# Kernel optimization log

Measured on AMD Instinct MI355X. Metric: run time of the kernel, lower is better.

Reference implementation:

```python
import jax, jax.numpy as jnp
import numpy as np

FEA, DK, H = 512, 64, 8
B, L = 4, 2048
EPS = 1e-5


def _layernorm(x, g, b):
    mu = jnp.mean(x, axis=-1, keepdims=True)
    var = jnp.mean(jnp.square(x - mu), axis=-1, keepdims=True)
    return (x - mu) * jax.lax.rsqrt(var + EPS) * g + b


def setup_inputs() -> dict:
    key = jax.random.key(0)
    ks = jax.random.split(key, 12)
    d = {
        'qx': jax.random.normal(ks[0], (B, L, FEA), jnp.float32),
        'kx': jax.random.normal(ks[1], (B, L, FEA), jnp.float32),
        'vx': jax.random.normal(ks[2], (B, L, FEA), jnp.float32),
        'maskPAD': jax.random.randint(ks[3], (B, L, L), 0, 2, jnp.int32),
        # attention projections (stored as [in, out]); biases zero-init as in module
        'wq': jax.random.normal(ks[4], (FEA, DK * H), jnp.float32) * 0.02,
        'bq': jnp.zeros((DK * H,), jnp.float32),
        'wk': jax.random.normal(ks[5], (FEA, DK * H), jnp.float32) * 0.02,
        'bk': jnp.zeros((DK * H,), jnp.float32),
        'wv': jax.random.normal(ks[6], (FEA, DK * H), jnp.float32) * 0.02,
        'bv': jnp.zeros((DK * H,), jnp.float32),
        'wo': jax.random.normal(ks[7], (DK * H, FEA), jnp.float32) * 0.02,
        'bo': jnp.zeros((FEA,), jnp.float32),
        # FFN
        'w1': jax.random.normal(ks[8], (FEA, 4 * FEA), jnp.float32) * 0.02,
        'b1': jnp.zeros((4 * FEA,), jnp.float32),
        'w2': jax.random.normal(ks[9], (4 * FEA, FEA), jnp.float32) * 0.02,
        'b2': jnp.zeros((FEA,), jnp.float32),
        # layer norms
        'ln1_g': jnp.ones((FEA,), jnp.float32),
        'ln1_b': jnp.zeros((FEA,), jnp.float32),
        'ln2_g': jnp.ones((FEA,), jnp.float32),
        'ln2_b': jnp.zeros((FEA,), jnp.float32),
    }
    return d


def reference(qx, kx, vx, maskPAD, wq, bq, wk, bk, wv, bv, wo, bo,
              w1, b1, w2, b2, ln1_g, ln1_b, ln2_g, ln2_b):
    b, l, _ = qx.shape
    # project and split heads: [B, H, L, DK]
    q = (qx @ wq + bq).reshape(b, l, H, DK).transpose(0, 2, 1, 3)
    k = (kx @ wk + bk).reshape(b, l, H, DK).transpose(0, 2, 1, 3)
    v = (vx @ wv + bv).reshape(b, l, H, DK).transpose(0, 2, 1, 3)
    scores = jnp.einsum('bhqd,bhkd->bhqk', q, k) / np.sqrt(DK)  # [B,H,L,L]
    mask = (maskPAD == 0)[:, None, :, :]
    scores = jnp.where(mask, jnp.float32(-2 ** 15 + 1), scores)
    alpha = jax.nn.softmax(scores, axis=-1)
    z = jnp.einsum('bhqk,bhkd->bhqd', alpha, v)  # [B,H,L,DK]
    z = z.transpose(0, 2, 1, 3).reshape(b, l, H * DK)
    z = z @ wo + bo
    # post-LN FFN block (dropout = identity at inference)
    zn = _layernorm(vx + z, ln1_g, ln1_b)
    ffn = jax.nn.gelu(zn @ w1 + b1, approximate=False) @ w2 + b2
    return _layernorm(zn + ffn, ln2_g, ln2_b)
```

## Files before the change

kernel.cpp:

```cpp
#include <hip/hip_runtime.h>
#include <cstdint>


typedef __bf16 bf16;
typedef __bf16 bf16x8 __attribute__((ext_vector_type(8)));
typedef float floatx4 __attribute__((ext_vector_type(4)));

__device__ __forceinline__ floatx4 mfma_bf16(bf16x8 a, bf16x8 b, floatx4 c) {
  return __builtin_amdgcn_mfma_f32_16x16x32_bf16(a, b, c, 0, 0, 0);
}

__device__ __forceinline__ void load_lds_16(const void* g, void* l) {
  auto gp = reinterpret_cast<const void __attribute__((address_space(1)))*>(
      reinterpret_cast<uintptr_t>(g));
  auto lp = reinterpret_cast<void __attribute__((address_space(3)))*>(
      (unsigned int)reinterpret_cast<uintptr_t>(l));
  __builtin_amdgcn_global_load_lds(gp, lp, 16, 0, 0);
}

__device__ __forceinline__ float gelu_f(float x) {
  float t = 0.7978845608f * (x + 0.044715f * x * x * x);
  float e = __builtin_amdgcn_exp2f(t * 2.885390082f);
  float th = 1.0f - 2.0f * __builtin_amdgcn_rcpf(e + 1.0f);
  return 0.5f * x * (1.0f + th);
}

#define PLANE128 2064
#define PLANE64 1040
#define PSTR 72

__global__ void __launch_bounds__(256) transpose4_k(const float* __restrict__ w0,
                                                    const float* __restrict__ w1,
                                                    const float* __restrict__ w2,
                                                    const float* __restrict__ w3,
                                                    bf16* __restrict__ o0,
                                                    bf16* __restrict__ o1,
                                                    bf16* __restrict__ o2,
                                                    bf16* __restrict__ o3) {
  const float* in = (blockIdx.z == 0) ? w0 : (blockIdx.z == 1) ? w1
                    : (blockIdx.z == 2) ? w2 : w3;
  bf16* out = (blockIdx.z == 0) ? o0 : (blockIdx.z == 1) ? o1
              : (blockIdx.z == 2) ? o2 : o3;
  __shared__ float tile[32][33];
  int m0 = blockIdx.x * 32, k0 = blockIdx.y * 32;
  int tx = threadIdx.x, ty = threadIdx.y;
  for (int i = ty; i < 32; i += 8)
    tile[i][tx] = in[(size_t)(k0 + i) * 512 + m0 + tx];
  __syncthreads();
  for (int i = ty; i < 32; i += 8)
    out[(size_t)(m0 + i) * 512 + k0 + tx] = (bf16)tile[tx][i];
}

__global__ void __launch_bounds__(256) transpose_k(const float* __restrict__ in,
                                                   bf16* __restrict__ out,
                                                   int K, int M) {
  __shared__ float tile[32][33];
  int m0 = blockIdx.x * 32, k0 = blockIdx.y * 32;
  int tx = threadIdx.x, ty = threadIdx.y;
  for (int i = ty; i < 32; i += 8)
    tile[i][tx] = in[(size_t)(k0 + i) * M + m0 + tx];
  __syncthreads();
  for (int i = ty; i < 32; i += 8)
    out[(size_t)(m0 + i) * K + k0 + tx] = (bf16)tile[tx][i];
}

__global__ void __launch_bounds__(256) maskbits_k(const int* __restrict__ m,
                                                  unsigned long long* __restrict__ out) {
  int w = blockIdx.x * 4 + (threadIdx.x >> 6);
  int lane = threadIdx.x & 63;
  int v = m[(size_t)w * 64 + lane];
  unsigned long long b = __ballot(v != 0);
  if (lane == 0) out[w] = b;
}

template <int EPI>
__device__ __forceinline__ void epi_store(void* Cout, int n, int m, int M,
                                          float val) {
  if constexpr (EPI == 1) {
    int bb = n >> 11, l = n & 2047, hh = m >> 6, d = m & 63;
    ((bf16*)Cout)[((size_t)((bb * 8 + hh) * 2048 + l)) * 64 + d] = (bf16)val;
  } else if constexpr (EPI == 2) {
    int bb = n >> 11, l = n & 2047, hh = m >> 6, d = m & 63;
    ((bf16*)Cout)[((size_t)((bb * 8 + hh) * 64 + d)) * 2048 + l] = (bf16)val;
  } else if constexpr (EPI == 3) {
    ((bf16*)Cout)[(size_t)n * M + m] = (bf16)gelu_f(val);
  } else if constexpr (EPI == 4) {
    ((float*)Cout)[(size_t)n * M + m] = val;
  } else {
    ((float*)Cout)[(size_t)n * M + m] += val;
  }
}

template <int EPI, bool TALL>
__global__ void __launch_bounds__(256) gemm_bt(const bf16* __restrict__ A,
                                               const bf16* __restrict__ Bt,
                                               const float* __restrict__ bias,
                                               void* __restrict__ Cout,
                                               int M, int K, int lda, int ldb) {
  __shared__ __attribute__((aligned(16))) char As[8 * PLANE128];
  __shared__ __attribute__((aligned(16))) char Bs[TALL ? 8 * PLANE64 : 8 * PLANE128];
  int tid = threadIdx.x, wave = tid >> 6, lane = tid & 63;
  int lrow = lane & 15, quad = lane >> 4;
  int n0 = blockIdx.y * 128;
  int m0 = blockIdx.x * (TALL ? 64 : 128);
  int wr = wave >> 1, wc = wave & 1;
  floatx4 zero4 = {0.f, 0.f, 0.f, 0.f};
  constexpr int NI = TALL ? 2 : 4;
  floatx4 acc[NI][4];
#pragma unroll
  for (int i = 0; i < NI; ++i)
#pragma unroll
    for (int j = 0; j < 4; ++j) acc[i][j] = zero4;
  for (int k0 = 0; k0 < K; k0 += 64) {
    __syncthreads();
#pragma unroll
    for (int h = 0; h < 2; ++h) {
      int p = wave + 4 * h;
#pragma unroll
      for (int j = 0; j < 2; ++j) {
        int row = j * 64 + lane;
        load_lds_16(A + (size_t)(n0 + row) * lda + k0 + p * 8,
                    As + p * PLANE128 + j * 1024 + lane * 16);
      }
      if constexpr (TALL) {
        load_lds_16(Bt + (size_t)(m0 + lane) * ldb + k0 + p * 8,
                    Bs + p * PLANE64 + lane * 16);
      } else {
#pragma unroll
        for (int j = 0; j < 2; ++j) {
          int row = j * 64 + lane;
          load_lds_16(Bt + (size_t)(m0 + row) * ldb + k0 + p * 8,
                      Bs + p * PLANE128 + j * 1024 + lane * 16);
        }
      }
    }
    __syncthreads();
#pragma unroll
    for (int h = 0; h < 2; ++h) {
      int pb = h * 4 + quad;
      bf16x8 af[NI], bfr[4];
#pragma unroll
      for (int i = 0; i < NI; ++i) {
        int row = (TALL ? wave * 32 : wr * 64) + i * 16 + lrow;
        af[i] = *(const bf16x8*)(As + pb * PLANE128 + row * 16);
      }
#pragma unroll
      for (int j = 0; j < 4; ++j) {
        if constexpr (TALL)
          bfr[j] = *(const bf16x8*)(Bs + pb * PLANE64 + (j * 16 + lrow) * 16);
        else
          bfr[j] = *(const bf16x8*)(Bs + pb * PLANE128 +
                                    (wc * 64 + j * 16 + lrow) * 16);
      }
#pragma unroll
      for (int i = 0; i < NI; ++i)
#pragma unroll
        for (int j = 0; j < 4; ++j)
          acc[i][j] = mfma_bf16(af[i], bfr[j], acc[i][j]);
    }
  }
  float bv[4];
#pragma unroll
  for (int j = 0; j < 4; ++j) {
    int m = m0 + (TALL ? 0 : wc * 64) + j * 16 + lrow;
    bv[j] = (EPI == 5) ? 0.f : bias[m];
  }
#pragma unroll
  for (int i = 0; i < NI; ++i)
#pragma unroll
    for (int j = 0; j < 4; ++j)
#pragma unroll
      for (int r = 0; r < 4; ++r) {
        int n = n0 + (TALL ? wave * 32 : wr * 64) + i * 16 + quad * 4 + r;
        int m = m0 + (TALL ? 0 : wc * 64) + j * 16 + lrow;
        epi_store<EPI>(Cout, n, m, M, acc[i][j][r] + bv[j]);
      }
}

__global__ void __launch_bounds__(256) qkv_k(const float* __restrict__ qx,
                                             const float* __restrict__ kx,
                                             const float* __restrict__ vx,
                                             const bf16* __restrict__ wqT,
                                             const bf16* __restrict__ wkT,
                                             const bf16* __restrict__ wvT,
                                             const float* __restrict__ bq,
                                             const float* __restrict__ bk,
                                             const float* __restrict__ bv_,
                                             bf16* __restrict__ qh,
                                             bf16* __restrict__ kh,
                                             bf16* __restrict__ vt) {
  __shared__ __attribute__((aligned(16))) char As[8 * PLANE128];
  __shared__ __attribute__((aligned(16))) char Bs[8 * PLANE128];
  int tid = threadIdx.x, wave = tid >> 6, lane = tid & 63;
  int lrow = lane & 15, quad = lane >> 4;
  int seg = blockIdx.y >> 6;
  int n0 = (blockIdx.y & 63) * 128, m0 = blockIdx.x * 128;
  const float* Af = (seg == 0) ? qx : (seg == 1) ? kx : vx;
  const bf16* Bt = (seg == 0) ? wqT : (seg == 1) ? wkT : wvT;
  const float* bias = (seg == 0) ? bq : (seg == 1) ? bk : bv_;
  bf16* out = (seg == 0) ? qh : (seg == 1) ? kh : vt;
  int wr = wave >> 1, wc = wave & 1;
  floatx4 zero4 = {0.f, 0.f, 0.f, 0.f};
  floatx4 acc[4][4];
#pragma unroll
  for (int i = 0; i < 4; ++i)
#pragma unroll
    for (int j = 0; j < 4; ++j) acc[i][j] = zero4;
  int arow = tid >> 2, ap = tid & 3;
  for (int k0 = 0; k0 < 512; k0 += 64) {
    bf16x8 a[4];
#pragma unroll
    for (int u = 0; u < 4; ++u) {
      int row = arow + (u & 1) * 64, p = ap + (u >> 1) * 4;
      const float* src = Af + (size_t)(n0 + row) * 512 + k0 + p * 8;
      float4 x0 = *(const float4*)src;
      float4 x1 = *(const float4*)(src + 4);
      a[u][0] = (bf16)x0.x; a[u][1] = (bf16)x0.y; a[u][2] = (bf16)x0.z;
      a[u][3] = (bf16)x0.w; a[u][4] = (bf16)x1.x; a[u][5] = (bf16)x1.y;
      a[u][6] = (bf16)x1.z; a[u][7] = (bf16)x1.w;
    }
    __syncthreads();
#pragma unroll
    for (int u = 0; u < 4; ++u) {
      int row = arow + (u & 1) * 64, p = ap + (u >> 1) * 4;
      *(bf16x8*)(As + p * PLANE128 + row * 16) = a[u];
    }
#pragma unroll
    for (int h = 0; h < 2; ++h) {
      int p = wave + 4 * h;
#pragma unroll
      for (int j = 0; j < 2; ++j) {
        int row = j * 64 + lane;
        load_lds_16(Bt + (size_t)(m0 + row) * 512 + k0 + p * 8,
                    Bs + p * PLANE128 + j * 1024 + lane * 16);
      }
    }
    __syncthreads();
#pragma unroll
    for (int h = 0; h < 2; ++h) {
      int pb = h * 4 + quad;
      bf16x8 af[4], bfr[4];
#pragma unroll
      for (int t = 0; t < 4; ++t) {
        af[t] = *(const bf16x8*)(As + pb * PLANE128 + (wr * 64 + t * 16 + lrow) * 16);
        bfr[t] = *(const bf16x8*)(Bs + pb * PLANE128 + (wc * 64 + t * 16 + lrow) * 16);
      }
#pragma unroll
      for (int i = 0; i < 4; ++i)
#pragma unroll
        for (int j = 0; j < 4; ++j) acc[i][j] = mfma_bf16(af[i], bfr[j], acc[i][j]);
    }
  }
  float bvv[4];
#pragma unroll
  for (int j = 0; j < 4; ++j) bvv[j] = bias[m0 + wc * 64 + j * 16 + lrow];
#pragma unroll
  for (int i = 0; i < 4; ++i)
#pragma unroll
    for (int j = 0; j < 4; ++j)
#pragma unroll
      for (int r = 0; r < 4; ++r) {
        int n = n0 + wr * 64 + i * 16 + quad * 4 + r;
        int m = m0 + wc * 64 + j * 16 + lrow;
        float val = acc[i][j][r] + bvv[j];
        int bb = n >> 11, l = n & 2047, hh = m >> 6, d = m & 63;
        if (seg == 2)
          out[((size_t)((bb * 8 + hh) * 64 + d)) * 2048 + l] = (bf16)val;
        else
          out[((size_t)((bb * 8 + hh) * 2048 + l)) * 64 + d] = (bf16)val;
      }
}

__global__ void __launch_bounds__(256) attn_k(const bf16* __restrict__ Qh,
                                              const bf16* __restrict__ Kh,
                                              const bf16* __restrict__ Vt,
                                              const unsigned long long* __restrict__ MB,
                                              bf16* __restrict__ Z) {
  __shared__ __attribute__((aligned(16))) char Ks[8 * PLANE64];
  __shared__ __attribute__((aligned(16))) char Vs[8 * PLANE64];
  __shared__ __attribute__((aligned(16))) bf16 Ps[4][16 * PSTR];
  int qt = blockIdx.x, h = blockIdx.y, b = blockIdx.z;
  int tid = threadIdx.x, wave = tid >> 6, lane = tid & 63;
  int lrow = lane & 15, quad = lane >> 4;
  int q0 = qt * 64;
  size_t headbase = (size_t)(b * 8 + h) * 2048 * 64;

  const bf16* Qp = Qh + headbase + (size_t)(q0 + wave * 16 + lrow) * 64 + quad * 8;
  bf16x8 qf0 = *(const bf16x8*)Qp;
  bf16x8 qf1 = *(const bf16x8*)(Qp + 32);

  floatx4 zero4 = {0.f, 0.f, 0.f, 0.f};
  floatx4 o_acc[4], acc_l = zero4;
#pragma unroll
  for (int dt = 0; dt < 4; ++dt) o_acc[dt] = zero4;
  bf16x8 ones;
#pragma unroll
  for (int j = 0; j < 8; ++j) ones[j] = (bf16)1.0f;

  const bf16* Vg = Vt + headbase;
  const uint2* MBb = (const uint2*)(MB + ((size_t)b * 2048 + q0 + wave * 16) * 32);
  bf16* Pw = Ps[wave];
  const float C = 0.1803368801f;

  for (int kt = 0; kt < 32; ++kt) {
    int kk0 = kt * 64;
    const bf16* Kg = Kh + headbase + (size_t)kk0 * 64;
    __syncthreads();
#pragma unroll
    for (int j = 0; j < 2; ++j) {
      int p = wave * 2 + j;
      load_lds_16(Kg + (size_t)lane * 64 + p * 8, Ks + p * PLANE64 + lane * 16);
      load_lds_16(Vg + (size_t)lane * 2048 + kk0 + p * 8,
                  Vs + p * PLANE64 + lane * 16);
    }
    unsigned sx[4], sy[4];
#pragma unroll
    for (int r = 0; r < 4; ++r) {
      uint2 mw = MBb[(quad * 4 + r) * 32 + kt];
      sx[r] = mw.x >> lrow;
      sy[r] = mw.y >> lrow;
    }
    __syncthreads();

#pragma unroll
    for (int nt = 0; nt < 4; ++nt) {
      int R = nt * 16 + lrow;
      bf16x8 k0f = *(const bf16x8*)(Ks + quad * PLANE64 + R * 16);
      bf16x8 k1f = *(const bf16x8*)(Ks + (quad + 4) * PLANE64 + R * 16);
      floatx4 aa = zero4;
      aa = mfma_bf16(qf0, k0f, aa);
      aa = mfma_bf16(qf1, k1f, aa);
#pragma unroll
      for (int r = 0; r < 4; ++r) {
        float e = __builtin_amdgcn_exp2f(aa[r] * C);
        unsigned bit = ((nt < 2 ? sx[r] : sy[r]) >> ((nt & 1) * 16)) & 1u;
        Pw[(quad * 4 + r) * PSTR + nt * 16 + lrow] = (bf16)(bit ? e : 0.f);
      }
    }
    bf16x8 pf0 = *(const bf16x8*)(Pw + lrow * PSTR + quad * 8);
    bf16x8 pf1 = *(const bf16x8*)(Pw + lrow * PSTR + 32 + quad * 8);
    acc_l = mfma_bf16(pf0, ones, acc_l);
    acc_l = mfma_bf16(pf1, ones, acc_l);
#pragma unroll
    for (int dt = 0; dt < 4; ++dt) {
      int R = dt * 16 + lrow;
      bf16x8 v0 = *(const bf16x8*)(Vs + quad * PLANE64 + R * 16);
      bf16x8 v1 = *(const bf16x8*)(Vs + (quad + 4) * PLANE64 + R * 16);
      o_acc[dt] = mfma_bf16(pf0, v0, o_acc[dt]);
      o_acc[dt] = mfma_bf16(pf1, v1, o_acc[dt]);
    }
  }
  float lr[4];
#pragma unroll
  for (int r = 0; r < 4; ++r) lr[r] = 1.0f / acc_l[r];
#pragma unroll
  for (int dt = 0; dt < 4; ++dt)
#pragma unroll
    for (int r = 0; r < 4; ++r) {
      int qrow = q0 + wave * 16 + quad * 4 + r;
      int d = dt * 16 + lrow;
      Z[((size_t)(b * 2048 + qrow)) * 512 + h * 64 + d] = (bf16)(o_acc[dt][r] * lr[r]);
    }
}

template <bool A_BF16, bool OUT_BF16>
__global__ void __launch_bounds__(256) ln_k(const void* __restrict__ a_,
                                            const float* __restrict__ s,
                                            const float* __restrict__ g,
                                            const float* __restrict__ bta,
                                            void* __restrict__ out_) {
  int row = blockIdx.x * 4 + (threadIdx.x >> 6);
  int lane = threadIdx.x & 63;
  size_t base = (size_t)row * 512 + lane * 8;
  float x[8];
  float4 sa = *(const float4*)(s + base);
  float4 sb = *(const float4*)(s + base + 4);
  if constexpr (A_BF16) {
    bf16x8 av = *(const bf16x8*)((const bf16*)a_ + base);
    x[0] = (float)av[0] + sa.x; x[1] = (float)av[1] + sa.y;
    x[2] = (float)av[2] + sa.z; x[3] = (float)av[3] + sa.w;
    x[4] = (float)av[4] + sb.x; x[5] = (float)av[5] + sb.y;
    x[6] = (float)av[6] + sb.z; x[7] = (float)av[7] + sb.w;
  } else {
    float4 a0 = *(const float4*)((const float*)a_ + base);
    float4 a1 = *(const float4*)((const float*)a_ + base + 4);
    x[0] = a0.x + sa.x; x[1] = a0.y + sa.y; x[2] = a0.z + sa.z; x[3] = a0.w + sa.w;
    x[4] = a1.x + sb.x; x[5] = a1.y + sb.y; x[6] = a1.z + sb.z; x[7] = a1.w + sb.w;
  }
  float sum = 0.f;
#pragma unroll
  for (int i = 0; i < 8; ++i) sum += x[i];
#pragma unroll
  for (int off = 1; off < 64; off <<= 1) sum += __shfl_xor(sum, off, 64);
  float mu = sum * (1.0f / 512.0f);
  float vs = 0.f;
#pragma unroll
  for (int i = 0; i < 8; ++i) { float d = x[i] - mu; vs += d * d; }
#pragma unroll
  for (int off = 1; off < 64; off <<= 1) vs += __shfl_xor(vs, off, 64);
  float rstd = rsqrtf(vs * (1.0f / 512.0f) + 1e-5f);
  float4 g0 = *(const float4*)(g + lane * 8);
  float4 g1 = *(const float4*)(g + lane * 8 + 4);
  float4 b0 = *(const float4*)(bta + lane * 8);
  float4 b1 = *(const float4*)(bta + lane * 8 + 4);
  float gg[8] = {g0.x, g0.y, g0.z, g0.w, g1.x, g1.y, g1.z, g1.w};
  float bb[8] = {b0.x, b0.y, b0.z, b0.w, b1.x, b1.y, b1.z, b1.w};
  if constexpr (OUT_BF16) {
    bf16x8 o;
#pragma unroll
    for (int i = 0; i < 8; ++i)
      o[i] = (bf16)((x[i] - mu) * rstd * gg[i] + bb[i]);
    *(bf16x8*)((bf16*)out_ + base) = o;
  } else {
    float4 o0, o1;
    o0.x = (x[0] - mu) * rstd * gg[0] + bb[0];
    o0.y = (x[1] - mu) * rstd * gg[1] + bb[1];
    o0.z = (x[2] - mu) * rstd * gg[2] + bb[2];
    o0.w = (x[3] - mu) * rstd * gg[3] + bb[3];
    o1.x = (x[4] - mu) * rstd * gg[4] + bb[4];
    o1.y = (x[5] - mu) * rstd * gg[5] + bb[5];
    o1.z = (x[6] - mu) * rstd * gg[6] + bb[6];
    o1.w = (x[7] - mu) * rstd * gg[7] + bb[7];
    *(float4*)((float*)out_ + base) = o0;
    *(float4*)((float*)out_ + base + 4) = o1;
  }
}

extern "C" void kernel_launch(void* const* d_in, const int* in_sizes, int n_in,
                              void* d_out, int out_size, void* d_ws, size_t ws_size,
                              hipStream_t stream) {
  const float* qx = (const float*)d_in[0];
  const float* kx = (const float*)d_in[1];
  const float* vx = (const float*)d_in[2];
  const int* maskPAD = (const int*)d_in[3];
  const float* wq = (const float*)d_in[4];
  const float* bq = (const float*)d_in[5];
  const float* wk = (const float*)d_in[6];
  const float* bk = (const float*)d_in[7];
  const float* wv = (const float*)d_in[8];
  const float* bv = (const float*)d_in[9];
  const float* wo = (const float*)d_in[10];
  const float* bo = (const float*)d_in[11];
  const float* w1 = (const float*)d_in[12];
  const float* b1 = (const float*)d_in[13];
  const float* w2 = (const float*)d_in[14];
  const float* b2 = (const float*)d_in[15];
  const float* g1 = (const float*)d_in[16];
  const float* be1 = (const float*)d_in[17];
  const float* g2 = (const float*)d_in[18];
  const float* be2 = (const float*)d_in[19];

  char* w = (char*)d_ws;
  size_t off = 0;
  auto alloc = [&](size_t bytes) {
    void* p = w + off;
    off += (bytes + 255) & ~(size_t)255;
    return p;
  };
  bf16* wqT = (bf16*)alloc(512 * 512 * 2);
  bf16* wkT = (bf16*)alloc(512 * 512 * 2);
  bf16* wvT = (bf16*)alloc(512 * 512 * 2);
  bf16* woT = (bf16*)alloc(512 * 512 * 2);
  bf16* w1T = (bf16*)alloc(2048 * 512 * 2);
  bf16* w2T = (bf16*)alloc(512 * 2048 * 2);
  unsigned long long* mbits = (unsigned long long*)alloc((size_t)4 * 2048 * 32 * 8);
  bf16* qh = (bf16*)alloc((size_t)8192 * 512 * 2);
  bf16* kh = (bf16*)alloc((size_t)8192 * 512 * 2);
  bf16* vt = (bf16*)alloc((size_t)8192 * 512 * 2);
  bf16* z = (bf16*)alloc((size_t)8192 * 512 * 2);
  float* s12 = (float*)qh;
  bf16* zn = vt;
  size_t h1_bytes = (size_t)8192 * 2048 * 2;
  bool big = (off + h1_bytes) <= ws_size;
  bf16* h1 = big ? (bf16*)alloc(h1_bytes) : z;

  dim3 tb(32, 8);
  transpose4_k<<<dim3(16, 16, 4), tb, 0, stream>>>(wq, wk, wv, wo, wqT, wkT, wvT, woT);
  transpose_k<<<dim3(64, 16), tb, 0, stream>>>(w1, w1T, 512, 2048);
  transpose_k<<<dim3(16, 64), tb, 0, stream>>>(w2, w2T, 2048, 512);
  maskbits_k<<<65536, 256, 0, stream>>>(maskPAD, mbits);
  qkv_k<<<dim3(4, 192), 256, 0, stream>>>(qx, kx, vx, wqT, wkT, wvT, bq, bk, bv,
                                          qh, kh, vt);
  attn_k<<<dim3(32, 8, 4), 256, 0, stream>>>(qh, kh, vt, mbits, z);
  gemm_bt<4, true><<<dim3(8, 64), 256, 0, stream>>>(z, woT, bo, s12, 512, 512,
                                                    512, 512);
  ln_k<false, true><<<2048, 256, 0, stream>>>(vx, s12, g1, be1, zn);
  if (big) {
    gemm_bt<3, false><<<dim3(16, 64), 256, 0, stream>>>(zn, w1T, b1, h1, 2048,
                                                        512, 512, 512);
    gemm_bt<4, true><<<dim3(8, 64), 256, 0, stream>>>(h1, w2T, b2, s12, 512,
                                                      2048, 2048, 2048);
  } else {
    for (int p = 0; p < 4; ++p) {
      gemm_bt<3, true><<<dim3(8, 64), 256, 0, stream>>>(
          zn, w1T + (size_t)p * 512 * 512, b1 + p * 512, h1, 512, 512, 512, 512);
      if (p == 0)
        gemm_bt<4, true><<<dim3(8, 64), 256, 0, stream>>>(
            h1, w2T + p * 512, b2, s12, 512, 512, 512, 2048);
      else
        gemm_bt<5, true><<<dim3(8, 64), 256, 0, stream>>>(
            h1, w2T + p * 512, nullptr, s12, 512, 512, 512, 2048);
    }
  }
  ln_k<true, false><<<2048, 256, 0, stream>>>(zn, s12, g2, be2, (float*)d_out);
}
```

Before: 455.0 us.

## Pre-convert QKV inputs to bf16 and transpose attention MFMA operand order

Adds a kernel that converts qx/kx/vx to bf16 once, so a new QKV GEMM can stream the A operand into LDS with direct global-to-LDS loads instead of converting fp32 on the fly. In attention, the MFMA operands are swapped so each lane holds a row of scores, which allows one 64-bit mask word load per lane, packed bf16x4 writes of P, and vectorized Z stores. This costs an extra conversion pass and a larger workspace, and the conversion path is used only when the workspace is big enough.

Result: slower. 469.1 us (+3.1%).

```diff
diff --git a/kernel.cpp b/kernel.cpp
--- a/kernel.cpp
+++ b/kernel.cpp
@@ -3,6 +3,7 @@
 
 
 typedef __bf16 bf16;
+typedef __bf16 bf16x4 __attribute__((ext_vector_type(4)));
 typedef __bf16 bf16x8 __attribute__((ext_vector_type(8)));
 typedef float floatx4 __attribute__((ext_vector_type(4)));
 
@@ -64,6 +65,19 @@
     out[(size_t)(m0 + i) * K + k0 + tx] = (bf16)tile[tx][i];
 }
 
+__global__ void __launch_bounds__(256) cvt3_k(const float* __restrict__ a,
+                                              const float* __restrict__ b,
+                                              const float* __restrict__ c,
+                                              bf16* __restrict__ out) {
+  int seg = blockIdx.x >> 12;
+  const float* in = (seg == 0) ? a : (seg == 1) ? b : c;
+  int i = ((blockIdx.x & 4095) * 256 + threadIdx.x) * 4;
+  float4 v = *(const float4*)(in + i);
+  bf16x4 o;
+  o[0] = (bf16)v.x; o[1] = (bf16)v.y; o[2] = (bf16)v.z; o[3] = (bf16)v.w;
+  *(bf16x4*)(out + (size_t)seg * 4194304 + i) = o;
+}
+
 __global__ void __launch_bounds__(256) maskbits_k(const int* __restrict__ m,
                                                   unsigned long long* __restrict__ out) {
   int w = blockIdx.x * 4 + (threadIdx.x >> 6);
@@ -174,6 +188,83 @@
         int n = n0 + (TALL ? wave * 32 : wr * 64) + i * 16 + quad * 4 + r;
         int m = m0 + (TALL ? 0 : wc * 64) + j * 16 + lrow;
         epi_store<EPI>(Cout, n, m, M, acc[i][j][r] + bv[j]);
+      }
+}
+
+__global__ void __launch_bounds__(256) qkv2_k(const bf16* __restrict__ xall,
+                                              const bf16* __restrict__ wqT,
+                                              const bf16* __restrict__ wkT,
+                                              const bf16* __restrict__ wvT,
+                                              const float* __restrict__ bq,
+                                              const float* __restrict__ bk,
+                                              const float* __restrict__ bv_,
+                                              bf16* __restrict__ qh,
+                                              bf16* __restrict__ kh,
+                                              bf16* __restrict__ vt) {
+  __shared__ __attribute__((aligned(16))) char As[8 * PLANE128];
+  __shared__ __attribute__((aligned(16))) char Bs[8 * PLANE128];
+  int tid = threadIdx.x, wave = tid >> 6, lane = tid & 63;
+  int lrow = lane & 15, quad = lane >> 4;
+  int seg = blockIdx.y >> 6;
+  int n0 = (blockIdx.y & 63) * 128, m0 = blockIdx.x * 128;
+  const bf16* A = xall + (size_t)seg * 4194304;
+  const bf16* Bt = (seg == 0) ? wqT : (seg == 1) ? wkT : wvT;
+  const float* bias = (seg == 0) ? bq : (seg == 1) ? bk : bv_;
+  bf16* out = (seg == 0) ? qh : (seg == 1) ? kh : vt;
+  int wr = wave >> 1, wc = wave & 1;
+  floatx4 zero4 = {0.f, 0.f, 0.f, 0.f};
+  floatx4 acc[4][4];
+#pragma unroll
+  for (int i = 0; i < 4; ++i)
+#pragma unroll
+    for (int j = 0; j < 4; ++j) acc[i][j] = zero4;
+  for (int k0 = 0; k0 < 512; k0 += 64) {
+    __syncthreads();
+#pragma unroll
+    for (int h = 0; h < 2; ++h) {
+      int p = wave + 4 * h;
+#pragma unroll
+      for (int j = 0; j < 2; ++j) {
+        int row = j * 64 + lane;
+        load_lds_16(A + (size_t)(n0 + row) * 512 + k0 + p * 8,
+                    As + p * PLANE128 + j * 1024 + lane * 16);
+        load_lds_16(Bt + (size_t)(m0 + row) * 512 + k0 + p * 8,
+                    Bs + p * PLANE128 + j * 1024 + lane * 16);
+      }
+    }
+    __syncthreads();
+#pragma unroll
+    for (int h = 0; h < 2; ++h) {
+      int pb = h * 4 + quad;
+      bf16x8 af[4], bfr[4];
+#pragma unroll
+      for (int t = 0; t < 4; ++t) {
+        af[t] = *(const bf16x8*)(As + pb * PLANE128 + (wr * 64 + t * 16 + lrow) * 16);
+        bfr[t] = *(const bf16x8*)(Bs + pb * PLANE128 + (wc * 64 + t * 16 + lrow) * 16);
+      }
+#pragma unroll
+      for (int i = 0; i < 4; ++i)
+#pragma unroll
+        for (int j = 0; j < 4; ++j) acc[i][j] = mfma_bf16(af[i], bfr[j], acc[i][j]);
+    }
+  }
+  float bvv[4];
+#pragma unroll
+  for (int j = 0; j < 4; ++j) bvv[j] = bias[m0 + wc * 64 + j * 16 + lrow];
+#pragma unroll
+  for (int i = 0; i < 4; ++i)
+#pragma unroll
+    for (int j = 0; j < 4; ++j)
+#pragma unroll
+      for (int r = 0; r < 4; ++r) {
+        int n = n0 + wr * 64 + i * 16 + quad * 4 + r;
+        int m = m0 + wc * 64 + j * 16 + lrow;
+        float val = acc[i][j][r] + bvv[j];
+        int bb = n >> 11, l = n & 2047, hh = m >> 6, d = m & 63;
+        if (seg == 2)
+          out[((size_t)((bb * 8 + hh) * 64 + d)) * 2048 + l] = (bf16)val;
+        else
+          out[((size_t)((bb * 8 + hh) * 2048 + l)) * 64 + d] = (bf16)val;
       }
 }
 
@@ -278,7 +369,7 @@
                                               bf16* __restrict__ Z) {
   __shared__ __attribute__((aligned(16))) char Ks[8 * PLANE64];
   __shared__ __attribute__((aligned(16))) char Vs[8 * PLANE64];
-  __shared__ __attribute__((aligned(16))) bf16 Ps[4][16 * PSTR];
+  __shared__ __attribute__((aligned(16))) bf16 Pt[4][16 * PSTR];
   int qt = blockIdx.x, h = blockIdx.y, b = blockIdx.z;
   int tid = threadIdx.x, wave = tid >> 6, lane = tid & 63;
   int lrow = lane & 15, quad = lane >> 4;
@@ -298,8 +389,9 @@
   for (int j = 0; j < 8; ++j) ones[j] = (bf16)1.0f;
 
   const bf16* Vg = Vt + headbase;
-  const uint2* MBb = (const uint2*)(MB + ((size_t)b * 2048 + q0 + wave * 16) * 32);
-  bf16* Pw = Ps[wave];
+  const unsigned long long* MBrow =
+      MB + ((size_t)b * 2048 + q0 + wave * 16 + lrow) * 32;
+  bf16* Pw = Pt[wave];
   const float C = 0.1803368801f;
 
   for (int kt = 0; kt < 32; ++kt) {
@@ -313,13 +405,9 @@
       load_lds_16(Vg + (size_t)lane * 2048 + kk0 + p * 8,
                   Vs + p * PLANE64 + lane * 16);
     }
-    unsigned sx[4], sy[4];
-#pragma unroll
-    for (int r = 0; r < 4; ++r) {
-      uint2 mw = MBb[(quad * 4 + r) * 32 + kt];
-      sx[r] = mw.x >> lrow;
-      sy[r] = mw.y >> lrow;
-    }
+    unsigned long long mw = MBrow[kt];
+    unsigned sx = (unsigned)(mw >> (quad * 4));
+    unsigned sy = (unsigned)(mw >> (32 + quad * 4));
     __syncthreads();
 
 #pragma unroll
@@ -328,39 +416,39 @@
       bf16x8 k0f = *(const bf16x8*)(Ks + quad * PLANE64 + R * 16);
       bf16x8 k1f = *(const bf16x8*)(Ks + (quad + 4) * PLANE64 + R * 16);
       floatx4 aa = zero4;
-      aa = mfma_bf16(qf0, k0f, aa);
-      aa = mfma_bf16(qf1, k1f, aa);
+      aa = mfma_bf16(k0f, qf0, aa);
+      aa = mfma_bf16(k1f, qf1, aa);
+      unsigned sel = (nt < 2 ? sx : sy) >> ((nt & 1) * 16);
+      bf16x4 pv;
 #pragma unroll
       for (int r = 0; r < 4; ++r) {
         float e = __builtin_amdgcn_exp2f(aa[r] * C);
-        unsigned bit = ((nt < 2 ? sx[r] : sy[r]) >> ((nt & 1) * 16)) & 1u;
-        Pw[(quad * 4 + r) * PSTR + nt * 16 + lrow] = (bf16)(bit ? e : 0.f);
-      }
+        pv[r] = (bf16)(((sel >> r) & 1u) ? e : 0.f);
+      }
+      *(bf16x4*)(Pw + lrow * PSTR + nt * 16 + quad * 4) = pv;
     }
     bf16x8 pf0 = *(const bf16x8*)(Pw + lrow * PSTR + quad * 8);
     bf16x8 pf1 = *(const bf16x8*)(Pw + lrow * PSTR + 32 + quad * 8);
-    acc_l = mfma_bf16(pf0, ones, acc_l);
-    acc_l = mfma_bf16(pf1, ones, acc_l);
+    acc_l = mfma_bf16(ones, pf0, acc_l);
+    acc_l = mfma_bf16(ones, pf1, acc_l);
 #pragma unroll
     for (int dt = 0; dt < 4; ++dt) {
       int R = dt * 16 + lrow;
       bf16x8 v0 = *(const bf16x8*)(Vs + quad * PLANE64 + R * 16);
       bf16x8 v1 = *(const bf16x8*)(Vs + (quad + 4) * PLANE64 + R * 16);
-      o_acc[dt] = mfma_bf16(pf0, v0, o_acc[dt]);
-      o_acc[dt] = mfma_bf16(pf1, v1, o_acc[dt]);
-    }
-  }
-  float lr[4];
-#pragma unroll
-  for (int r = 0; r < 4; ++r) lr[r] = 1.0f / acc_l[r];
-#pragma unroll
-  for (int dt = 0; dt < 4; ++dt)
-#pragma unroll
-    for (int r = 0; r < 4; ++r) {
-      int qrow = q0 + wave * 16 + quad * 4 + r;
-      int d = dt * 16 + lrow;
-      Z[((size_t)(b * 2048 + qrow)) * 512 + h * 64 + d] = (bf16)(o_acc[dt][r] * lr[r]);
-    }
+      o_acc[dt] = mfma_bf16(v0, pf0, o_acc[dt]);
+      o_acc[dt] = mfma_bf16(v1, pf1, o_acc[dt]);
+    }
+  }
+  float lr = __builtin_amdgcn_rcpf(acc_l[0]);
+  size_t zrow = ((size_t)(b * 2048 + q0 + wave * 16 + lrow)) * 512 + h * 64;
+#pragma unroll
+  for (int dt = 0; dt < 4; ++dt) {
+    bf16x4 ov;
+#pragma unroll
+    for (int r = 0; r < 4; ++r) ov[r] = (bf16)(o_acc[dt][r] * lr);
+    *(bf16x4*)(Z + zrow + dt * 16 + quad * 4) = ov;
+  }
 }
 
 template <bool A_BF16, bool OUT_BF16>
@@ -464,12 +552,23 @@
   bf16* w1T = (bf16*)alloc(2048 * 512 * 2);
   bf16* w2T = (bf16*)alloc(512 * 2048 * 2);
   unsigned long long* mbits = (unsigned long long*)alloc((size_t)4 * 2048 * 32 * 8);
-  bf16* qh = (bf16*)alloc((size_t)8192 * 512 * 2);
-  bf16* kh = (bf16*)alloc((size_t)8192 * 512 * 2);
-  bf16* vt = (bf16*)alloc((size_t)8192 * 512 * 2);
-  bf16* z = (bf16*)alloc((size_t)8192 * 512 * 2);
-  float* s12 = (float*)qh;
-  bf16* zn = vt;
+  size_t xall_bytes = (size_t)3 * 8192 * 512 * 2;
+  size_t act4 = (size_t)8192 * 512 * 2;
+  bool fast = (off + xall_bytes + 4 * (act4 + 256)) <= ws_size;
+  bf16* xall = fast ? (bf16*)alloc(xall_bytes) : nullptr;
+  bf16* qh = (bf16*)alloc(act4);
+  bf16* kh = (bf16*)alloc(act4);
+  bf16* vt = (bf16*)alloc(act4);
+  bf16* z = (bf16*)alloc(act4);
+  float* s12;
+  bf16* zn;
+  if (fast) {
+    s12 = (float*)xall;
+    zn = (bf16*)((char*)xall + (size_t)8192 * 512 * 4);
+  } else {
+    s12 = (float*)qh;
+    zn = vt;
+  }
   size_t h1_bytes = (size_t)8192 * 2048 * 2;
   bool big = (off + h1_bytes) <= ws_size;
   bf16* h1 = big ? (bf16*)alloc(h1_bytes) : z;
@@ -479,8 +578,14 @@
   transpose_k<<<dim3(64, 16), tb, 0, stream>>>(w1, w1T, 512, 2048);
   transpose_k<<<dim3(16, 64), tb, 0, stream>>>(w2, w2T, 2048, 512);
   maskbits_k<<<65536, 256, 0, stream>>>(maskPAD, mbits);
-  qkv_k<<<dim3(4, 192), 256, 0, stream>>>(qx, kx, vx, wqT, wkT, wvT, bq, bk, bv,
-                                          qh, kh, vt);
+  if (fast) {
+    cvt3_k<<<12288, 256, 0, stream>>>(qx, kx, vx, xall);
+    qkv2_k<<<dim3(4, 192), 256, 0, stream>>>(xall, wqT, wkT, wvT, bq, bk, bv,
+                                             qh, kh, vt);
+  } else {
+    qkv_k<<<dim3(4, 192), 256, 0, stream>>>(qx, kx, vx, wqT, wkT, wvT, bq, bk,
+                                            bv, qh, kh, vt);
+  }
   attn_k<<<dim3(32, 8, 4), 256, 0, stream>>>(qh, kh, vt, mbits, z);
   gemm_bt<4, true><<<dim3(8, 64), 256, 0, stream>>>(z, woT, bo, s12, 512, 512,
                                                     512, 512);
```
